# Kernel tuning notes

Hardware: AMD Instinct MI355X
Metric: run time of the kernel (lower is better)

## Reference

```python
import jax, jax.numpy as jnp
import numpy as np

N_HEADS = 12
HIDDEN = 768
HEAD_DIM = HIDDEN // N_HEADS
B, S = 4, 2048


def setup_inputs() -> dict:
    key = jax.random.key(0)
    ks = jax.random.split(key, 7)
    bound = 1.0 / np.sqrt(HIDDEN)  # torch nn.Linear default init range
    inputs = jax.random.normal(ks[0], (B, S, HIDDEN), dtype=jnp.float32)
    Wq = jax.random.uniform(ks[1], (HIDDEN, HIDDEN), jnp.float32, -bound, bound)
    bq = jax.random.uniform(ks[2], (HIDDEN,), jnp.float32, -bound, bound)
    Wk = jax.random.uniform(ks[3], (HIDDEN, HIDDEN), jnp.float32, -bound, bound)
    bk = jax.random.uniform(ks[4], (HIDDEN,), jnp.float32, -bound, bound)
    Wv = jax.random.uniform(ks[5], (HIDDEN, HIDDEN), jnp.float32, -bound, bound)
    bv = jax.random.uniform(ks[6], (HIDDEN,), jnp.float32, -bound, bound)
    return {"inputs": inputs, "Wq": Wq, "bq": bq, "Wk": Wk, "bk": bk, "Wv": Wv, "bv": bv}


def reference(inputs, Wq, bq, Wk, bk, Wv, bv):
    b, s, d = inputs.shape
    h, hd = N_HEADS, HEAD_DIM
    # torch Linear: x @ W^T + b; reshape to (b, s, h, hd) -> (b, h, s, hd)
    def proj(W, bias):
        y = inputs @ W.T + bias
        return y.reshape(b, s, h, hd).transpose(0, 2, 1, 3)
    q = proj(Wq, bq)
    k = proj(Wk, bk)
    v = proj(Wv, bv)
    scale = 1.0 / jnp.sqrt(jnp.asarray(hd, inputs.dtype))
    scores = jnp.einsum('bhqd,bhkd->bhqk', q, k) * scale  # [b,h,s,s] materialized as in source
    attn = jax.nn.softmax(scores, axis=-1)
    out = jnp.einsum('bhqk,bhkd->bhqd', attn, v)
    # (b, h, s, hd) -> (b, s, h*hd)
    return out.transpose(0, 2, 1, 3).reshape(b, s, d)
```

## Files before the change

### kernel.cpp

```cpp
#include <hip/hip_runtime.h>
#include <hip/hip_bf16.h>
#include <math.h>

#define NH   12
#define HD   64
#define HID  768
#define NB   4
#define SS   2048
#define MR   (NB*SS)

#define NXE  (MR*HID)
#define NWE  (HID*HID)

typedef unsigned short u16;
typedef u16   u16x8  __attribute__((ext_vector_type(8)));
typedef __bf16 bf16x8 __attribute__((ext_vector_type(8)));
typedef float f32x4  __attribute__((ext_vector_type(4)));

__device__ __forceinline__ u16 f2b(float f) {
    union { float f; unsigned i; } c; c.f = f;
    unsigned x = c.i + 0x7fffu + ((c.i >> 16) & 1u);
    return (u16)(x >> 16);
}
__device__ __forceinline__ unsigned pk2(float lo, float hi) {
    float2 f; f.x = lo; f.y = hi;
    union { __hip_bfloat162 h; unsigned u; } c;
    c.h = __float22bfloat162_rn(f);
    return c.u;
}
__device__ __forceinline__ f32x4 mfma16(u16x8 a, u16x8 b, f32x4 c) {
    return __builtin_amdgcn_mfma_f32_16x16x32_bf16(
        __builtin_bit_cast(bf16x8, a), __builtin_bit_cast(bf16x8, b), c, 0, 0, 0);
}
__device__ __forceinline__ void g2l16(const u16* g, u16* l) {
    __builtin_amdgcn_global_load_lds(
        (const __attribute__((address_space(1))) void*)g,
        (__attribute__((address_space(3))) void*)l, 16, 0, 0);
}
__device__ __forceinline__ int kperm(int k) {
    return ((k >> 5) << 5) | (((k >> 2) & 1) << 4) | (((k >> 3) & 3) << 2) | (k & 3);
}


__global__ __launch_bounds__(256) void to_bf16(
    const float* __restrict__ x,  const float* __restrict__ Wq,
    const float* __restrict__ Wk, const float* __restrict__ Wv,
    u16* __restrict__ dst)
{
    const int NX4 = NXE / 4, NW4 = NWE / 4, NT4 = NX4 + 3 * NW4;
    for (int i = blockIdx.x * 256 + threadIdx.x; i < NT4; i += gridDim.x * 256) {
        const float* src; u16* d;
        if (i < NX4) { src = x + (size_t)i * 4; d = dst + (size_t)i * 4; }
        else {
            int j = i - NX4; int w = j / NW4; int r = j - w * NW4;
            const float* Ws = (w == 0) ? Wq : ((w == 1) ? Wk : Wv);
            src = Ws + (size_t)r * 4; d = dst + NXE + (size_t)w * NWE + (size_t)r * 4;
        }
        float4 f = *(const float4*)src;
        uint2 o; o.x = pk2(f.x, f.y); o.y = pk2(f.z, f.w);
        *(uint2*)d = o;
    }
}

__global__ __launch_bounds__(256, 3) void qkv_proj(
    const u16* __restrict__ xb, const u16* __restrict__ Wb,
    const float* __restrict__ bq, const float* __restrict__ bk,
    const float* __restrict__ bv, u16* __restrict__ qkv)
{
    const int wsel = blockIdx.z;
    const u16* W = Wb + (size_t)wsel * NWE;
    const float* bias = (wsel == 0) ? bq : ((wsel == 1) ? bk : bv);
    u16* out = qkv + (size_t)wsel * MR * HID;

    const int m0 = blockIdx.x * 128, n0 = blockIdx.y * 128;
    __shared__ __align__(16) u16 smem[18432];

    const int tid  = threadIdx.x;
    const int lane = tid & 63, wid = tid >> 6;
    const int quad = lane >> 4, l16 = lane & 15;
    const int wm = wid >> 1, wn = wid & 1;
    const int qsw = quad ^ ((l16 >> 1) & 3);

    const int rA = 2 * wid * 16 + (lane >> 2);
    const int colh = 8 * ((lane & 3) ^ ((lane >> 3) & 3));
    const u16* gx0 = xb + (size_t)(m0 + rA) * HID + colh;
    const u16* gx1 = gx0 + (size_t)16 * HID;
    const u16* gw0 = W  + (size_t)(n0 + rA) * HID + colh;
    const u16* gw1 = gw0 + (size_t)16 * HID;
    u16* lA = smem + (2 * wid) * 512 + lane * 8;

    f32x4 acc[4][4] = {};

    for (int k0 = 0; k0 < HID; k0 += 64) {
        g2l16(gx0 + k0,      lA);            g2l16(gx1 + k0,      lA + 512);
        g2l16(gx0 + k0 + 32, lA + 4096);     g2l16(gx1 + k0 + 32, lA + 4608);
        g2l16(gw0 + k0,      lA + 8192);     g2l16(gw1 + k0,      lA + 8704);
        g2l16(gw0 + k0 + 32, lA + 12288);    g2l16(gw1 + k0 + 32, lA + 12800);
        __syncthreads();
        #pragma unroll
        for (int hh = 0; hh < 2; hh++) {
            u16x8 af[4], bf[4];
            #pragma unroll
            for (int i = 0; i < 4; i++)
                af[i] = *(const u16x8*)(smem + hh * 4096 + (wm * 64 + i * 16 + l16) * 32 + qsw * 8);
            #pragma unroll
            for (int j = 0; j < 4; j++)
                bf[j] = *(const u16x8*)(smem + 8192 + hh * 4096 + (wn * 64 + j * 16 + l16) * 32 + qsw * 8);
            #pragma unroll
            for (int i = 0; i < 4; i++)
                #pragma unroll
                for (int j = 0; j < 4; j++)
                    acc[i][j] = mfma16(af[i], bf[j], acc[i][j]);
        }
        __syncthreads();
    }

    if (wsel == 2) {
        u16* lt = smem + wid * 4608;
        #pragma unroll
        for (int j = 0; j < 4; j++) {
            const int col = n0 + wn * 64 + j * 16 + l16;
            const float bb = bias[col];
            #pragma unroll
            for (int i = 0; i < 4; i++) {
                uint2 pk;
                pk.x = pk2(acc[i][j][0] + bb, acc[i][j][1] + bb);
                pk.y = pk2(acc[i][j][2] + bb, acc[i][j][3] + bb);
                *(uint2*)(lt + (j * 16 + l16) * 72 + i * 16 + quad * 4) = pk;
            }
        }
        __syncthreads();
        const int bidx = m0 >> 11;
        const int s0 = (m0 & 2047) + wm * 64;
        #pragma unroll
        for (int it = 0; it < 8; it++) {
            const int dl = it * 8 + (lane >> 3), sl = (lane & 7) * 8;
            uint4 w = *(const uint4*)(lt + dl * 72 + sl);
            const int col = n0 + wn * 64 + dl;
            const int hh = col >> 6, d = col & 63;
            *(uint4*)(out + ((size_t)(bidx * NH + hh) * HD + d) * SS + s0 + sl) = w;
        }
    } else {
        const float scale = (wsel == 0) ? 0.18033688f : 1.0f;
        #pragma unroll
        for (int j = 0; j < 4; j++) {
            const int col = n0 + wn * 64 + j * 16 + l16;
            const float bb = bias[col];
            #pragma unroll
            for (int i = 0; i < 4; i++)
                #pragma unroll
                for (int r = 0; r < 4; r++) {
                    int row = m0 + wm * 64 + i * 16 + quad * 4 + r;
                    if (wsel == 1) row = (row & ~63) | kperm(row & 63);
                    out[(size_t)row * HID + col] = f2b((acc[i][j][r] + bb) * scale);
                }
        }
    }
}

__global__ __launch_bounds__(256, 3) void attn(
    const u16* __restrict__ qkv, float* __restrict__ out)
{
    const int lin = blockIdx.x;
    const int rx  = lin & 7;
    const int gg  = lin >> 3;
    const int qt  = gg & 15;
    const int bh  = rx * 6 + (gg >> 4);
    const int b   = bh / NH, h = bh - b * NH;
    const int q0  = qt * 128;

    const u16* qb  = qkv + (size_t)b * SS * HID + h * HD;
    const u16* kb  = qkv + (size_t)MR * HID + (size_t)b * SS * HID + h * HD;
    const u16* vtb = qkv + (size_t)2 * MR * HID + ((size_t)(b * NH + h) * HD) * SS;
    float*     ob  = out + (size_t)b * SS * HID + h * HD;

    __shared__ __align__(16) u16 KS[2][2][2048];
    __shared__ __align__(16) u16 VS[2][2][2048];

    const int tid  = threadIdx.x;
    const int lane = tid & 63, wid = tid >> 6;
    const int quad = lane >> 4, l16 = lane & 15;
    const int qsw = quad ^ ((l16 >> 1) & 3);

    const int srow = 16 * wid + (lane >> 2);
    const int sc8  = 8 * ((lane & 3) ^ ((lane >> 3) & 3));
    const int ldst = wid * 512 + lane * 8;

    u16x8 qf[2][2];
    #pragma unroll
    for (int t = 0; t < 2; t++) {
        const int row = q0 + t * 64 + wid * 16 + l16;
        #pragma unroll
        for (int hh = 0; hh < 2; hh++)
            qf[t][hh] = *(const u16x8*)(qb + (size_t)row * HID + hh * 32 + quad * 8);
    }

    u16x8 ones;
    #pragma unroll
    for (int e = 0; e < 8; e++) ones[e] = 0x3F80;

    f32x4 o2[2][4] = {};
    f32x4 lacc[2] = {};

    {
        const u16* kg = kb + (size_t)srow * HID + sc8;
        const u16* vg = vtb + (size_t)srow * SS + sc8;
        g2l16(kg, &KS[0][0][0] + ldst);  g2l16(kg + 32, &KS[0][1][0] + ldst);
        g2l16(vg, &VS[0][0][0] + ldst);  g2l16(vg + 32, &VS[0][1][0] + ldst);
    }
    __syncthreads();

    for (int kt = 0; kt < SS / 64; kt++) {
        const int cur = kt & 1;

        if (kt < 31) {
            const int kn = (kt + 1) * 64;
            const u16* kg = kb + (size_t)(kn + srow) * HID + sc8;
            const u16* vg = vtb + (size_t)srow * SS + kn + sc8;
            g2l16(kg, &KS[cur ^ 1][0][0] + ldst);  g2l16(kg + 32, &KS[cur ^ 1][1][0] + ldst);
            g2l16(vg, &VS[cur ^ 1][0][0] + ldst);  g2l16(vg + 32, &VS[cur ^ 1][1][0] + ldst);
        }

        u16x8 kf[4][2];
        #pragma unroll
        for (int n = 0; n < 4; n++)
            #pragma unroll
            for (int hh = 0; hh < 2; hh++)
                kf[n][hh] = *(const u16x8*)(&KS[cur][hh][0] + (n * 16 + l16) * 32 + qsw * 8);

        unsigned pkd[2][4][2];
        __builtin_amdgcn_s_setprio(1);
        #pragma unroll
        for (int t = 0; t < 2; t++)
            #pragma unroll
            for (int n = 0; n < 4; n++) {
                f32x4 s = {-6.f, -6.f, -6.f, -6.f};
                s = mfma16(kf[n][0], qf[t][0], s);
                s = mfma16(kf[n][1], qf[t][1], s);
                const float p0 = __builtin_amdgcn_exp2f(s[0]);
                const float p1 = __builtin_amdgcn_exp2f(s[1]);
                const float p2 = __builtin_amdgcn_exp2f(s[2]);
                const float p3 = __builtin_amdgcn_exp2f(s[3]);
                pkd[t][n][0] = pk2(p0, p1);
                pkd[t][n][1] = pk2(p2, p3);
            }
        __builtin_amdgcn_s_setprio(0);

        u16x8 vf[4][2];
        #pragma unroll
        for (int n2 = 0; n2 < 4; n2++)
            #pragma unroll
            for (int hh = 0; hh < 2; hh++)
                vf[n2][hh] = *(const u16x8*)(&VS[cur][hh][0] + (n2 * 16 + l16) * 32 + qsw * 8);

        __builtin_amdgcn_s_setprio(1);
        #pragma unroll
        for (int t = 0; t < 2; t++) {
            union { u16x8 v; unsigned d[4]; } bf0, bf1;
            bf0.d[0] = pkd[t][0][0]; bf0.d[1] = pkd[t][0][1];
            bf0.d[2] = pkd[t][1][0]; bf0.d[3] = pkd[t][1][1];
            bf1.d[0] = pkd[t][2][0]; bf1.d[1] = pkd[t][2][1];
            bf1.d[2] = pkd[t][3][0]; bf1.d[3] = pkd[t][3][1];
            lacc[t] = mfma16(ones, bf0.v, lacc[t]);
            lacc[t] = mfma16(ones, bf1.v, lacc[t]);
            #pragma unroll
            for (int n2 = 0; n2 < 4; n2++) {
                o2[t][n2] = mfma16(vf[n2][0], bf0.v, o2[t][n2]);
                o2[t][n2] = mfma16(vf[n2][1], bf1.v, o2[t][n2]);
            }
        }
        __builtin_amdgcn_s_setprio(0);
        __syncthreads();
    }

    #pragma unroll
    for (int t = 0; t < 2; t++) {
        const float inv = 1.f / lacc[t][0];
        const int q = q0 + t * 64 + wid * 16 + l16;
        #pragma unroll
        for (int n2 = 0; n2 < 4; n2++) {
            f32x4 w = o2[t][n2];
            w[0] *= inv; w[1] *= inv; w[2] *= inv; w[3] *= inv;
            *(f32x4*)(ob + (size_t)q * HID + n2 * 16 + quad * 4) = w;
        }
    }
}

extern "C" void kernel_launch(void* const* d_in, const int* in_sizes, int n_in,
                              void* d_out, int out_size, void* d_ws, size_t ws_size,
                              hipStream_t stream) {
    const float* x  = (const float*)d_in[0];
    const float* Wq = (const float*)d_in[1];
    const float* bq = (const float*)d_in[2];
    const float* Wk = (const float*)d_in[3];
    const float* bk = (const float*)d_in[4];
    const float* Wv = (const float*)d_in[5];
    const float* bv = (const float*)d_in[6];
    float* out = (float*)d_out;
    u16* qkv = (u16*)d_ws;
    u16* cvt = (u16*)d_out;

    to_bf16<<<1024, 256, 0, stream>>>(x, Wq, Wk, Wv, cvt);

    dim3 gp(MR / 128, HID / 128, 3);
    qkv_proj<<<gp, 256, 0, stream>>>(cvt, cvt + NXE, bq, bk, bv, qkv);

    attn<<<768, 256, 0, stream>>>(qkv, out);
}
```

Measured before the change: 185.0 us.

## Triple-buffer LDS staging with vmcnt waits and one barrier per step

Both the QKV projection GEMM and the attention kernel now use a three-stage LDS ring. Loads are issued two stages ahead and gated by explicit s_waitcnt vmcnt plus a single s_barrier per iteration, replacing the two __syncthreads per step. The GEMM now steps over 32-wide K slices instead of 64-wide ones. The goal is to hide global-to-LDS latency behind MFMA work and cut barrier stalls. In exchange LDS use grows (48KB for the GEMM, 48KB for attention), which could lower occupancy at launch_bounds 3, and correctness depends on the vmcnt counts matching the number of outstanding loads per stage.

```diff
diff --git a/kernel.cpp b/kernel.cpp
--- a/kernel.cpp
+++ b/kernel.cpp
@@ -73,7 +73,7 @@
     u16* out = qkv + (size_t)wsel * MR * HID;
 
     const int m0 = blockIdx.x * 128, n0 = blockIdx.y * 128;
-    __shared__ __align__(16) u16 smem[18432];
+    __shared__ __align__(16) u16 smem[24576];
 
     const int tid  = threadIdx.x;
     const int lane = tid & 63, wid = tid >> 6;
@@ -83,39 +83,54 @@
 
     const int rA = 2 * wid * 16 + (lane >> 2);
     const int colh = 8 * ((lane & 3) ^ ((lane >> 3) & 3));
-    const u16* gx0 = xb + (size_t)(m0 + rA) * HID + colh;
-    const u16* gx1 = gx0 + (size_t)16 * HID;
-    const u16* gw0 = W  + (size_t)(n0 + rA) * HID + colh;
-    const u16* gw1 = gw0 + (size_t)16 * HID;
+    const u16* gx = xb + (size_t)(m0 + rA) * HID + colh;
+    const u16* gw = W  + (size_t)(n0 + rA) * HID + colh;
     u16* lA = smem + (2 * wid) * 512 + lane * 8;
 
+#define QSTAGE(h, b) do {                                              \
+        const u16* ga_ = gx + 32 * (h);                                \
+        const u16* gb_ = gw + 32 * (h);                                \
+        u16* la_ = lA + (b) * 4096;                                    \
+        g2l16(ga_,            la_);                                    \
+        g2l16(ga_ + 16 * HID, la_ + 512);                              \
+        g2l16(gb_,            la_ + 12288);                            \
+        g2l16(gb_ + 16 * HID, la_ + 12800);                            \
+    } while (0)
+
     f32x4 acc[4][4] = {};
 
-    for (int k0 = 0; k0 < HID; k0 += 64) {
-        g2l16(gx0 + k0,      lA);            g2l16(gx1 + k0,      lA + 512);
-        g2l16(gx0 + k0 + 32, lA + 4096);     g2l16(gx1 + k0 + 32, lA + 4608);
-        g2l16(gw0 + k0,      lA + 8192);     g2l16(gw1 + k0,      lA + 8704);
-        g2l16(gw0 + k0 + 32, lA + 12288);    g2l16(gw1 + k0 + 32, lA + 12800);
+    QSTAGE(0, 0);
+    QSTAGE(1, 1);
+
+    #pragma unroll 3
+    for (int h = 0; h < 24; h++) {
+        const int cur = h % 3, nb = (h + 2) % 3;
+        if (h < 23) asm volatile("s_waitcnt vmcnt(4)" ::: "memory");
+        else        asm volatile("s_waitcnt vmcnt(0)" ::: "memory");
+        __builtin_amdgcn_s_barrier();
+        if (h + 2 < 24) QSTAGE(h + 2, nb);
+
+        const u16* Ab = smem + cur * 4096;
+        const u16* Bb = smem + 12288 + cur * 4096;
+        u16x8 af[4], bf[4];
+        #pragma unroll
+        for (int i = 0; i < 4; i++)
+            af[i] = *(const u16x8*)(Ab + (wm * 64 + i * 16 + l16) * 32 + qsw * 8);
+        #pragma unroll
+        for (int j = 0; j < 4; j++)
+            bf[j] = *(const u16x8*)(Bb + (wn * 64 + j * 16 + l16) * 32 + qsw * 8);
+        __builtin_amdgcn_s_setprio(1);
+        #pragma unroll
+        for (int i = 0; i < 4; i++)
+            #pragma unroll
+            for (int j = 0; j < 4; j++)
+                acc[i][j] = mfma16(af[i], bf[j], acc[i][j]);
+        __builtin_amdgcn_s_setprio(0);
+    }
+#undef QSTAGE
+
+    if (wsel == 2) {
         __syncthreads();
-        #pragma unroll
-        for (int hh = 0; hh < 2; hh++) {
-            u16x8 af[4], bf[4];
-            #pragma unroll
-            for (int i = 0; i < 4; i++)
-                af[i] = *(const u16x8*)(smem + hh * 4096 + (wm * 64 + i * 16 + l16) * 32 + qsw * 8);
-            #pragma unroll
-            for (int j = 0; j < 4; j++)
-                bf[j] = *(const u16x8*)(smem + 8192 + hh * 4096 + (wn * 64 + j * 16 + l16) * 32 + qsw * 8);
-            #pragma unroll
-            for (int i = 0; i < 4; i++)
-                #pragma unroll
-                for (int j = 0; j < 4; j++)
-                    acc[i][j] = mfma16(af[i], bf[j], acc[i][j]);
-        }
-        __syncthreads();
-    }
-
-    if (wsel == 2) {
         u16* lt = smem + wid * 4608;
         #pragma unroll
         for (int j = 0; j < 4; j++) {
@@ -174,8 +189,8 @@
     const u16* vtb = qkv + (size_t)2 * MR * HID + ((size_t)(b * NH + h) * HD) * SS;
     float*     ob  = out + (size_t)b * SS * HID + h * HD;
 
-    __shared__ __align__(16) u16 KS[2][2][2048];
-    __shared__ __align__(16) u16 VS[2][2][2048];
+    __shared__ __align__(16) u16 KS[3][2][2048];
+    __shared__ __align__(16) u16 VS[3][2][2048];
 
     const int tid  = threadIdx.x;
     const int lane = tid & 63, wid = tid >> 6;
@@ -186,6 +201,18 @@
     const int sc8  = 8 * ((lane & 3) ^ ((lane >> 3) & 3));
     const int ldst = wid * 512 + lane * 8;
 
+    const u16* kg = kb + (size_t)srow * HID + sc8;
+    const u16* vg = vtb + (size_t)srow * SS + sc8;
+
+#define ASTAGE(kt, bf_) do {                                            \
+        const u16* k_ = kg + (size_t)(kt) * 64 * HID;                   \
+        const u16* v_ = vg + (kt) * 64;                                 \
+        g2l16(k_,      &KS[(bf_)][0][0] + ldst);                        \
+        g2l16(k_ + 32, &KS[(bf_)][1][0] + ldst);                        \
+        g2l16(v_,      &VS[(bf_)][0][0] + ldst);                        \
+        g2l16(v_ + 32, &VS[(bf_)][1][0] + ldst);                        \
+    } while (0)
+
     u16x8 qf[2][2];
     #pragma unroll
     for (int t = 0; t < 2; t++) {
@@ -202,31 +229,26 @@
     f32x4 o2[2][4] = {};
     f32x4 lacc[2] = {};
 
-    {
-        const u16* kg = kb + (size_t)srow * HID + sc8;
-        const u16* vg = vtb + (size_t)srow * SS + sc8;
-        g2l16(kg, &KS[0][0][0] + ldst);  g2l16(kg + 32, &KS[0][1][0] + ldst);
-        g2l16(vg, &VS[0][0][0] + ldst);  g2l16(vg + 32, &VS[0][1][0] + ldst);
-    }
-    __syncthreads();
+    ASTAGE(0, 0);
+    ASTAGE(1, 1);
 
     for (int kt = 0; kt < SS / 64; kt++) {
-        const int cur = kt & 1;
-
-        if (kt < 31) {
-            const int kn = (kt + 1) * 64;
-            const u16* kg = kb + (size_t)(kn + srow) * HID + sc8;
-            const u16* vg = vtb + (size_t)srow * SS + kn + sc8;
-            g2l16(kg, &KS[cur ^ 1][0][0] + ldst);  g2l16(kg + 32, &KS[cur ^ 1][1][0] + ldst);
-            g2l16(vg, &VS[cur ^ 1][0][0] + ldst);  g2l16(vg + 32, &VS[cur ^ 1][1][0] + ldst);
-        }
+        const int cur = kt % 3, nb = (kt + 2) % 3;
+
+        if (kt < 31) asm volatile("s_waitcnt vmcnt(4)" ::: "memory");
+        else         asm volatile("s_waitcnt vmcnt(0)" ::: "memory");
+        __builtin_amdgcn_s_barrier();
+        if (kt + 2 < 32) ASTAGE(kt + 2, nb);
+
+        const u16* ksb = &KS[cur][0][0];
+        const u16* vsb = &VS[cur][0][0];
 
         u16x8 kf[4][2];
         #pragma unroll
         for (int n = 0; n < 4; n++)
             #pragma unroll
             for (int hh = 0; hh < 2; hh++)
-                kf[n][hh] = *(const u16x8*)(&KS[cur][hh][0] + (n * 16 + l16) * 32 + qsw * 8);
+                kf[n][hh] = *(const u16x8*)(ksb + hh * 2048 + (n * 16 + l16) * 32 + qsw * 8);
 
         unsigned pkd[2][4][2];
         __builtin_amdgcn_s_setprio(1);
@@ -251,7 +273,7 @@
         for (int n2 = 0; n2 < 4; n2++)
             #pragma unroll
             for (int hh = 0; hh < 2; hh++)
-                vf[n2][hh] = *(const u16x8*)(&VS[cur][hh][0] + (n2 * 16 + l16) * 32 + qsw * 8);
+                vf[n2][hh] = *(const u16x8*)(vsb + hh * 2048 + (n2 * 16 + l16) * 32 + qsw * 8);
 
         __builtin_amdgcn_s_setprio(1);
         #pragma unroll
@@ -270,8 +292,8 @@
             }
         }
         __builtin_amdgcn_s_setprio(0);
-        __syncthreads();
-    }
+    }
+#undef ASTAGE
 
     #pragma unroll
     for (int t = 0; t < 2; t++) {
```

Measured after the change: 192.8 us. +4.2%, slower.

## Software-pipeline attention loop with triple-buffered K/V and deferred PV

Applied to the files above, without the earlier changes.

Moves the K/V shared-memory staging from double to triple buffering with explicit vmcnt waits, so loads run two tiles ahead. It also skews the loop so the QK^T and exp of tile kt overlap with the PV and row-sum MFMAs of tile kt-1, ping-ponging the packed probabilities between two register sets, and adds an epilogue for the final PV step. This is meant to hide global-load latency and the MFMA-to-exp dependency. In exchange it uses more LDS and registers, which may reduce occupancy at launch bounds of 3 blocks per CU.

```diff
diff --git a/kernel.cpp b/kernel.cpp
--- a/kernel.cpp
+++ b/kernel.cpp
@@ -174,8 +174,8 @@
     const u16* vtb = qkv + (size_t)2 * MR * HID + ((size_t)(b * NH + h) * HD) * SS;
     float*     ob  = out + (size_t)b * SS * HID + h * HD;
 
-    __shared__ __align__(16) u16 KS[2][2][2048];
-    __shared__ __align__(16) u16 VS[2][2][2048];
+    __shared__ __align__(16) u16 KS[3][2][2048];
+    __shared__ __align__(16) u16 VS[3][2][2048];
 
     const int tid  = threadIdx.x;
     const int lane = tid & 63, wid = tid >> 6;
@@ -186,6 +186,18 @@
     const int sc8  = 8 * ((lane & 3) ^ ((lane >> 3) & 3));
     const int ldst = wid * 512 + lane * 8;
 
+    const u16* kg = kb + (size_t)srow * HID + sc8;
+    const u16* vg = vtb + (size_t)srow * SS + sc8;
+
+#define ASTAGE(kt, bf_) do {                                            \
+        const u16* k_ = kg + (size_t)(kt) * 64 * HID;                   \
+        const u16* v_ = vg + (kt) * 64;                                 \
+        g2l16(k_,      &KS[(bf_)][0][0] + ldst);                        \
+        g2l16(k_ + 32, &KS[(bf_)][1][0] + ldst);                        \
+        g2l16(v_,      &VS[(bf_)][0][0] + ldst);                        \
+        g2l16(v_ + 32, &VS[(bf_)][1][0] + ldst);                        \
+    } while (0)
+
     u16x8 qf[2][2];
     #pragma unroll
     for (int t = 0; t < 2; t++) {
@@ -202,75 +214,100 @@
     f32x4 o2[2][4] = {};
     f32x4 lacc[2] = {};
 
+    unsigned pkdA[2][4][2], pkdB[2][4][2];
+    #pragma unroll
+    for (int t = 0; t < 2; t++)
+        #pragma unroll
+        for (int n = 0; n < 4; n++) { pkdB[t][n][0] = 0u; pkdB[t][n][1] = 0u; }
+
+    ASTAGE(0, 0);
+    ASTAGE(1, 1);
+
+#define ABODY(kt, PKC, PKP) do {                                              \
+    const int cur_ = (kt) % 3;                                                \
+    const int prv_ = ((kt) == 0) ? 0 : ((kt) - 1) % 3;                        \
+    if ((kt) < 31) asm volatile("s_waitcnt vmcnt(4)" ::: "memory");           \
+    else           asm volatile("s_waitcnt vmcnt(0)" ::: "memory");           \
+    __builtin_amdgcn_s_barrier();                                             \
+    const u16* ksb_ = &KS[cur_][0][0];                                        \
+    const u16* vsb_ = &VS[prv_][0][0];                                        \
+    u16x8 kf_[4][2];                                                          \
+    _Pragma("unroll")                                                         \
+    for (int n_ = 0; n_ < 4; n_++)                                            \
+        _Pragma("unroll")                                                     \
+        for (int hh_ = 0; hh_ < 2; hh_++)                                     \
+            kf_[n_][hh_] = *(const u16x8*)(ksb_ + hh_ * 2048 + (n_ * 16 + l16) * 32 + qsw * 8); \
+    u16x8 vf_[4][2];                                                          \
+    _Pragma("unroll")                                                         \
+    for (int n_ = 0; n_ < 4; n_++)                                            \
+        _Pragma("unroll")                                                     \
+        for (int hh_ = 0; hh_ < 2; hh_++)                                     \
+            vf_[n_][hh_] = *(const u16x8*)(vsb_ + hh_ * 2048 + (n_ * 16 + l16) * 32 + qsw * 8); \
+    __builtin_amdgcn_s_setprio(1);                                            \
+    _Pragma("unroll")                                                         \
+    for (int t_ = 0; t_ < 2; t_++)                                            \
+        _Pragma("unroll")                                                     \
+        for (int n_ = 0; n_ < 4; n_++) {                                      \
+            f32x4 s_ = {-6.f, -6.f, -6.f, -6.f};                              \
+            s_ = mfma16(kf_[n_][0], qf[t_][0], s_);                           \
+            s_ = mfma16(kf_[n_][1], qf[t_][1], s_);                           \
+            PKC[t_][n_][0] = pk2(__builtin_amdgcn_exp2f(s_[0]),               \
+                                 __builtin_amdgcn_exp2f(s_[1]));              \
+            PKC[t_][n_][1] = pk2(__builtin_amdgcn_exp2f(s_[2]),               \
+                                 __builtin_amdgcn_exp2f(s_[3]));              \
+        }                                                                     \
+    _Pragma("unroll")                                                         \
+    for (int t_ = 0; t_ < 2; t_++) {                                          \
+        union { u16x8 v; unsigned d[4]; } b0_, b1_;                           \
+        b0_.d[0] = PKP[t_][0][0]; b0_.d[1] = PKP[t_][0][1];                   \
+        b0_.d[2] = PKP[t_][1][0]; b0_.d[3] = PKP[t_][1][1];                   \
+        b1_.d[0] = PKP[t_][2][0]; b1_.d[1] = PKP[t_][2][1];                   \
+        b1_.d[2] = PKP[t_][3][0]; b1_.d[3] = PKP[t_][3][1];                   \
+        lacc[t_] = mfma16(ones, b0_.v, lacc[t_]);                             \
+        lacc[t_] = mfma16(ones, b1_.v, lacc[t_]);                             \
+        _Pragma("unroll")                                                     \
+        for (int n_ = 0; n_ < 4; n_++) {                                      \
+            o2[t_][n_] = mfma16(vf_[n_][0], b0_.v, o2[t_][n_]);               \
+            o2[t_][n_] = mfma16(vf_[n_][1], b1_.v, o2[t_][n_]);               \
+        }                                                                     \
+    }                                                                         \
+    __builtin_amdgcn_s_setprio(0);                                            \
+    if ((kt) + 2 < 32) {                                                      \
+        __builtin_amdgcn_s_barrier();                                         \
+        ASTAGE((kt) + 2, ((kt) + 2) % 3);                                     \
+    }                                                                         \
+} while (0)
+
+    for (int k2 = 0; k2 < 16; k2++) {
+        ABODY(2 * k2,     pkdA, pkdB);
+        ABODY(2 * k2 + 1, pkdB, pkdA);
+    }
+#undef ABODY
+#undef ASTAGE
+
     {
-        const u16* kg = kb + (size_t)srow * HID + sc8;
-        const u16* vg = vtb + (size_t)srow * SS + sc8;
-        g2l16(kg, &KS[0][0][0] + ldst);  g2l16(kg + 32, &KS[0][1][0] + ldst);
-        g2l16(vg, &VS[0][0][0] + ldst);  g2l16(vg + 32, &VS[0][1][0] + ldst);
-    }
-    __syncthreads();
-
-    for (int kt = 0; kt < SS / 64; kt++) {
-        const int cur = kt & 1;
-
-        if (kt < 31) {
-            const int kn = (kt + 1) * 64;
-            const u16* kg = kb + (size_t)(kn + srow) * HID + sc8;
-            const u16* vg = vtb + (size_t)srow * SS + kn + sc8;
-            g2l16(kg, &KS[cur ^ 1][0][0] + ldst);  g2l16(kg + 32, &KS[cur ^ 1][1][0] + ldst);
-            g2l16(vg, &VS[cur ^ 1][0][0] + ldst);  g2l16(vg + 32, &VS[cur ^ 1][1][0] + ldst);
-        }
-
-        u16x8 kf[4][2];
-        #pragma unroll
-        for (int n = 0; n < 4; n++)
+        const u16* vsb_ = &VS[1][0][0];
+        u16x8 vf_[4][2];
+        #pragma unroll
+        for (int n2 = 0; n2 < 4; n2++)
             #pragma unroll
             for (int hh = 0; hh < 2; hh++)
-                kf[n][hh] = *(const u16x8*)(&KS[cur][hh][0] + (n * 16 + l16) * 32 + qsw * 8);
-
-        unsigned pkd[2][4][2];
-        __builtin_amdgcn_s_setprio(1);
-        #pragma unroll
-        for (int t = 0; t < 2; t++)
-            #pragma unroll
-            for (int n = 0; n < 4; n++) {
-                f32x4 s = {-6.f, -6.f, -6.f, -6.f};
-                s = mfma16(kf[n][0], qf[t][0], s);
-                s = mfma16(kf[n][1], qf[t][1], s);
-                const float p0 = __builtin_amdgcn_exp2f(s[0]);
-                const float p1 = __builtin_amdgcn_exp2f(s[1]);
-                const float p2 = __builtin_amdgcn_exp2f(s[2]);
-                const float p3 = __builtin_amdgcn_exp2f(s[3]);
-                pkd[t][n][0] = pk2(p0, p1);
-                pkd[t][n][1] = pk2(p2, p3);
+                vf_[n2][hh] = *(const u16x8*)(vsb_ + hh * 2048 + (n2 * 16 + l16) * 32 + qsw * 8);
+        #pragma unroll
+        for (int t = 0; t < 2; t++) {
+            union { u16x8 v; unsigned d[4]; } b0_, b1_;
+            b0_.d[0] = pkdB[t][0][0]; b0_.d[1] = pkdB[t][0][1];
+            b0_.d[2] = pkdB[t][1][0]; b0_.d[3] = pkdB[t][1][1];
+            b1_.d[0] = pkdB[t][2][0]; b1_.d[1] = pkdB[t][2][1];
+            b1_.d[2] = pkdB[t][3][0]; b1_.d[3] = pkdB[t][3][1];
+            lacc[t] = mfma16(ones, b0_.v, lacc[t]);
+            lacc[t] = mfma16(ones, b1_.v, lacc[t]);
+            #pragma unroll
+            for (int n2 = 0; n2 < 4; n2++) {
+                o2[t][n2] = mfma16(vf_[n2][0], b0_.v, o2[t][n2]);
+                o2[t][n2] = mfma16(vf_[n2][1], b1_.v, o2[t][n2]);
             }
-        __builtin_amdgcn_s_setprio(0);
-
-        u16x8 vf[4][2];
-        #pragma unroll
-        for (int n2 = 0; n2 < 4; n2++)
-            #pragma unroll
-            for (int hh = 0; hh < 2; hh++)
-                vf[n2][hh] = *(const u16x8*)(&VS[cur][hh][0] + (n2 * 16 + l16) * 32 + qsw * 8);
-
-        __builtin_amdgcn_s_setprio(1);
-        #pragma unroll
-        for (int t = 0; t < 2; t++) {
-            union { u16x8 v; unsigned d[4]; } bf0, bf1;
-            bf0.d[0] = pkd[t][0][0]; bf0.d[1] = pkd[t][0][1];
-            bf0.d[2] = pkd[t][1][0]; bf0.d[3] = pkd[t][1][1];
-            bf1.d[0] = pkd[t][2][0]; bf1.d[1] = pkd[t][2][1];
-            bf1.d[2] = pkd[t][3][0]; bf1.d[3] = pkd[t][3][1];
-            lacc[t] = mfma16(ones, bf0.v, lacc[t]);
-            lacc[t] = mfma16(ones, bf1.v, lacc[t]);
-            #pragma unroll
-            for (int n2 = 0; n2 < 4; n2++) {
-                o2[t][n2] = mfma16(vf[n2][0], bf0.v, o2[t][n2]);
-                o2[t][n2] = mfma16(vf[n2][1], bf1.v, o2[t][n2]);
-            }
-        }
-        __builtin_amdgcn_s_setprio(0);
-        __syncthreads();
+        }
     }
 
     #pragma unroll
```

After: 256.1 us. +38.4%, slower.

## Halve attention query tile to 64 rows and double grid size

Applied to the files above, without the earlier changes.

Each attention block now handles 64 query rows instead of 128, so the grid doubles to 1536 blocks and per-thread accumulators and Q fragments are halved. Launch bounds are raised to target 5 blocks per SIMD, aiming for more occupancy and better load balance across CUs. The cost is that every K/V tile is loaded from global memory into LDS twice as often per query row, and each block does less MFMA work per synchronization.

```diff
diff --git a/kernel.cpp b/kernel.cpp
--- a/kernel.cpp
+++ b/kernel.cpp
@@ -158,16 +158,16 @@
     }
 }
 
-__global__ __launch_bounds__(256, 3) void attn(
+__global__ __launch_bounds__(256, 5) void attn(
     const u16* __restrict__ qkv, float* __restrict__ out)
 {
     const int lin = blockIdx.x;
     const int rx  = lin & 7;
     const int gg  = lin >> 3;
-    const int qt  = gg & 15;
-    const int bh  = rx * 6 + (gg >> 4);
+    const int qt  = gg & 31;
+    const int bh  = rx * 6 + (gg >> 5);
     const int b   = bh / NH, h = bh - b * NH;
-    const int q0  = qt * 128;
+    const int q0  = qt * 64;
 
     const u16* qb  = qkv + (size_t)b * SS * HID + h * HD;
     const u16* kb  = qkv + (size_t)MR * HID + (size_t)b * SS * HID + h * HD;
@@ -186,25 +186,25 @@
     const int sc8  = 8 * ((lane & 3) ^ ((lane >> 3) & 3));
     const int ldst = wid * 512 + lane * 8;
 
-    u16x8 qf[2][2];
-    #pragma unroll
-    for (int t = 0; t < 2; t++) {
-        const int row = q0 + t * 64 + wid * 16 + l16;
+    const u16* kg = kb + (size_t)srow * HID + sc8;
+    const u16* vg = vtb + (size_t)srow * SS + sc8;
+
+    u16x8 qf[2];
+    {
+        const int row = q0 + wid * 16 + l16;
         #pragma unroll
         for (int hh = 0; hh < 2; hh++)
-            qf[t][hh] = *(const u16x8*)(qb + (size_t)row * HID + hh * 32 + quad * 8);
+            qf[hh] = *(const u16x8*)(qb + (size_t)row * HID + hh * 32 + quad * 8);
     }
 
     u16x8 ones;
     #pragma unroll
     for (int e = 0; e < 8; e++) ones[e] = 0x3F80;
 
-    f32x4 o2[2][4] = {};
-    f32x4 lacc[2] = {};
+    f32x4 o2[4] = {};
+    f32x4 lacc = {};
 
     {
-        const u16* kg = kb + (size_t)srow * HID + sc8;
-        const u16* vg = vtb + (size_t)srow * SS + sc8;
         g2l16(kg, &KS[0][0][0] + ldst);  g2l16(kg + 32, &KS[0][1][0] + ldst);
         g2l16(vg, &VS[0][0][0] + ldst);  g2l16(vg + 32, &VS[0][1][0] + ldst);
     }
@@ -215,10 +215,12 @@
 
         if (kt < 31) {
             const int kn = (kt + 1) * 64;
-            const u16* kg = kb + (size_t)(kn + srow) * HID + sc8;
-            const u16* vg = vtb + (size_t)srow * SS + kn + sc8;
-            g2l16(kg, &KS[cur ^ 1][0][0] + ldst);  g2l16(kg + 32, &KS[cur ^ 1][1][0] + ldst);
-            g2l16(vg, &VS[cur ^ 1][0][0] + ldst);  g2l16(vg + 32, &VS[cur ^ 1][1][0] + ldst);
+            const u16* k_ = kg + (size_t)kn * HID;
+            const u16* v_ = vg + kn;
+            g2l16(k_,      &KS[cur ^ 1][0][0] + ldst);
+            g2l16(k_ + 32, &KS[cur ^ 1][1][0] + ldst);
+            g2l16(v_,      &VS[cur ^ 1][0][0] + ldst);
+            g2l16(v_ + 32, &VS[cur ^ 1][1][0] + ldst);
         }
 
         u16x8 kf[4][2];
@@ -228,22 +230,20 @@
             for (int hh = 0; hh < 2; hh++)
                 kf[n][hh] = *(const u16x8*)(&KS[cur][hh][0] + (n * 16 + l16) * 32 + qsw * 8);
 
-        unsigned pkd[2][4][2];
+        unsigned pkd[4][2];
         __builtin_amdgcn_s_setprio(1);
         #pragma unroll
-        for (int t = 0; t < 2; t++)
-            #pragma unroll
-            for (int n = 0; n < 4; n++) {
-                f32x4 s = {-6.f, -6.f, -6.f, -6.f};
-                s = mfma16(kf[n][0], qf[t][0], s);
-                s = mfma16(kf[n][1], qf[t][1], s);
-                const float p0 = __builtin_amdgcn_exp2f(s[0]);
-                const float p1 = __builtin_amdgcn_exp2f(s[1]);
-                const float p2 = __builtin_amdgcn_exp2f(s[2]);
-                const float p3 = __builtin_amdgcn_exp2f(s[3]);
-                pkd[t][n][0] = pk2(p0, p1);
-                pkd[t][n][1] = pk2(p2, p3);
-            }
+        for (int n = 0; n < 4; n++) {
+            f32x4 s = {-6.f, -6.f, -6.f, -6.f};
+            s = mfma16(kf[n][0], qf[0], s);
+            s = mfma16(kf[n][1], qf[1], s);
+            const float p0 = __builtin_amdgcn_exp2f(s[0]);
+            const float p1 = __builtin_amdgcn_exp2f(s[1]);
+            const float p2 = __builtin_amdgcn_exp2f(s[2]);
+            const float p3 = __builtin_amdgcn_exp2f(s[3]);
+            pkd[n][0] = pk2(p0, p1);
+            pkd[n][1] = pk2(p2, p3);
+        }
         __builtin_amdgcn_s_setprio(0);
 
         u16x8 vf[4][2];
@@ -254,32 +254,30 @@
                 vf[n2][hh] = *(const u16x8*)(&VS[cur][hh][0] + (n2 * 16 + l16) * 32 + qsw * 8);
 
         __builtin_amdgcn_s_setprio(1);
-        #pragma unroll
-        for (int t = 0; t < 2; t++) {
+        {
             union { u16x8 v; unsigned d[4]; } bf0, bf1;
-            bf0.d[0] = pkd[t][0][0]; bf0.d[1] = pkd[t][0][1];
-            bf0.d[2] = pkd[t][1][0]; bf0.d[3] = pkd[t][1][1];
-            bf1.d[0] = pkd[t][2][0]; bf1.d[1] = pkd[t][2][1];
-            bf1.d[2] = pkd[t][3][0]; bf1.d[3] = pkd[t][3][1];
-            lacc[t] = mfma16(ones, bf0.v, lacc[t]);
-            lacc[t] = mfma16(ones, bf1.v, lacc[t]);
+            bf0.d[0] = pkd[0][0]; bf0.d[1] = pkd[0][1];
+            bf0.d[2] = pkd[1][0]; bf0.d[3] = pkd[1][1];
+            bf1.d[0] = pkd[2][0]; bf1.d[1] = pkd[2][1];
+            bf1.d[2] = pkd[3][0]; bf1.d[3] = pkd[3][1];
+            lacc = mfma16(ones, bf0.v, lacc);
+            lacc = mfma16(ones, bf1.v, lacc);
             #pragma unroll
             for (int n2 = 0; n2 < 4; n2++) {
-                o2[t][n2] = mfma16(vf[n2][0], bf0.v, o2[t][n2]);
-                o2[t][n2] = mfma16(vf[n2][1], bf1.v, o2[t][n2]);
+                o2[n2] = mfma16(vf[n2][0], bf0.v, o2[n2]);
+                o2[n2] = mfma16(vf[n2][1], bf1.v, o2[n2]);
             }
         }
         __builtin_amdgcn_s_setprio(0);
         __syncthreads();
     }
 
-    #pragma unroll
-    for (int t = 0; t < 2; t++) {
-        const float inv = 1.f / lacc[t][0];
-        const int q = q0 + t * 64 + wid * 16 + l16;
+    {
+        const float inv = 1.f / lacc[0];
+        const int q = q0 + wid * 16 + l16;
         #pragma unroll
         for (int n2 = 0; n2 < 4; n2++) {
-            f32x4 w = o2[t][n2];
+            f32x4 w = o2[n2];
             w[0] *= inv; w[1] *= inv; w[2] *= inv; w[3] *= inv;
             *(f32x4*)(ob + (size_t)q * HID + n2 * 16 + quad * 4) = w;
         }
@@ -305,5 +303,5 @@
     dim3 gp(MR / 128, HID / 128, 3);
     qkv_proj<<<gp, 256, 0, stream>>>(cvt, cvt + NXE, bq, bk, bv, qkv);
 
-    attn<<<768, 256, 0, stream>>>(qkv, out);
-}
+    attn<<<1536, 256, 0, stream>>>(qkv, out);
+}
```

New measurement: 196.2 us. +6.0%, slower.
